# Performance work log

Hardware: AMD Instinct MI355X
Metric: run time of the kernel (lower is better)

Reference implementation:

```python
import jax, jax.numpy as jnp
import numpy as np

N_NODES = 100000
N_EDGES = 1600000
IN_DIM, HID_DIM, OUT_DIM = 128, 64, 16
BN_EPS = 1e-5


def sage_conv(x, edge_index, W_l, b_l, W_r):
    # PyG SAGEConv (aggr='mean'): out = lin_l(mean_j x_j) + lin_r(x_i)
    src, dst = edge_index[0], edge_index[1]
    msgs = x[src]                                   # [E, F] gather
    sums = jax.ops.segment_sum(msgs, dst, num_segments=N_NODES)      # [N, F]
    cnt = jax.ops.segment_sum(jnp.ones((src.shape[0],), x.dtype), dst,
                              num_segments=N_NODES)                  # [N]
    agg = sums / jnp.maximum(cnt, 1.0)[:, None]     # mean; 0 for isolated nodes
    return agg @ W_l.T + b_l + x @ W_r.T


def batchnorm(x, gamma, beta):
    # BatchNorm1d in training mode: normalize over the node (batch) axis
    mean = jnp.mean(x, axis=0)
    var = jnp.var(x, axis=0)
    return (x - mean) * jax.lax.rsqrt(var + BN_EPS) * gamma + beta


def setup_inputs() -> dict:
    key = jax.random.key(0)
    ks = jax.random.split(key, 8)
    x = jax.random.normal(ks[0], (N_NODES, IN_DIM), dtype=jnp.float32)
    edge_index = jax.random.randint(ks[1], (2, N_EDGES), 0, N_NODES)
    s1 = 1.0 / np.sqrt(IN_DIM)
    s2 = 1.0 / np.sqrt(HID_DIM)
    return {
        "x": x,
        "edge_index": edge_index,
        "W1_l": jax.random.uniform(ks[2], (HID_DIM, IN_DIM), minval=-s1, maxval=s1),
        "b1": jnp.zeros((HID_DIM,), jnp.float32),
        "W1_r": jax.random.uniform(ks[3], (HID_DIM, IN_DIM), minval=-s1, maxval=s1),
        "bn_gamma": jnp.ones((HID_DIM,), jnp.float32),
        "bn_beta": jnp.zeros((HID_DIM,), jnp.float32),
        "W2_l": jax.random.uniform(ks[4], (OUT_DIM, HID_DIM), minval=-s2, maxval=s2),
        "b2": jnp.zeros((OUT_DIM,), jnp.float32),
        "W2_r": jax.random.uniform(ks[5], (OUT_DIM, HID_DIM), minval=-s2, maxval=s2),
    }


def reference(x, edge_index, W1_l, b1, W1_r, bn_gamma, bn_beta, W2_l, b2, W2_r):
    h = sage_conv(x, edge_index, W1_l, b1, W1_r)
    h = jax.nn.relu(batchnorm(h, bn_gamma, bn_beta))
    return sage_conv(h, edge_index, W2_l, b2, W2_r)
```

## Files before the change

kernel.cpp:

```cpp
#include <hip/hip_runtime.h>

#define NN 100000
#define NE 1600000
#define NPB 128
#define NBK 782
#define EPB 16384
#define NPART 98
#define NCVT 18
#define NTILES 1563
#define CAP 4096

#define OFF_H      0
#define OFF_GCNT   0
#define OFF_GOFS   80000
#define OFF_W1BF   160000
#define OFF_YL     6400000
#define OFF_YR     9600000
#define OFF_EBUF   12800000
#define OFF_HIST   14400000
#define OFF_BSTART 14500000
#define OFF_BNACC  14500800
#define OFF_W2BF   14500928

typedef __attribute__((ext_vector_type(8))) short bf16x8;
typedef __attribute__((ext_vector_type(4))) float f32x4;

__device__ __forceinline__ ushort f2bf(float f) {
  unsigned u = __float_as_uint(f);
  u += 0x7fffu + ((u >> 16) & 1);
  return (ushort)(u >> 16);
}
#define BFLO(u) __uint_as_float(((u) & 0xffffu) << 16)
#define BFHI(u) __uint_as_float((u) & 0xffff0000u)

__global__ __launch_bounds__(1024) void k_bcnt2(const int* __restrict__ ei,
                                                int* __restrict__ gcnt,
                                                const float* __restrict__ W1l,
                                                const float* __restrict__ W1r,
                                                const float* __restrict__ W2l,
                                                const float* __restrict__ W2r,
                                                ushort* __restrict__ w1bf,
                                                ushort* __restrict__ w2bf) {
  const int tid = threadIdx.x;
  if (blockIdx.x >= NPART) {
    int i = (blockIdx.x - NPART) * 1024 + tid;
    if (i < 16384) {
      w1bf[i] = f2bf(i < 8192 ? W1l[i] : W1r[i - 8192]);
    } else if (i < 16384 + 2048) {
      int j = i - 16384;
      w2bf[j] = f2bf(j < 1024 ? W2l[j] : W2r[j - 1024]);
    }
    return;
  }
  __shared__ int cnt[NBK];
  for (int i = tid; i < NBK; i += 1024) cnt[i] = 0;
  __syncthreads();
  int e0 = blockIdx.x * EPB;
  int e1 = min(e0 + EPB, NE);
  for (int e = e0 + tid; e < e1; e += 1024)
    atomicAdd(&cnt[ei[NE + e] >> 7], 1);
  __syncthreads();
  for (int b = tid; b < NBK; b += 1024)
    gcnt[blockIdx.x * NBK + b] = cnt[b];
}

__global__ __launch_bounds__(1024) void k_bprep(const int* __restrict__ gcnt,
                                                int* __restrict__ bstart,
                                                int* __restrict__ gofs) {
  __shared__ int sd[1024];
  int t = threadIdx.x;
  int total = 0;
  if (t < NBK)
    for (int blk = 0; blk < NPART; ++blk) total += gcnt[blk * NBK + t];
  sd[t] = total;
  __syncthreads();
  for (int off = 1; off < 1024; off <<= 1) {
    int u = (t >= off) ? sd[t - off] : 0;
    __syncthreads();
    sd[t] += u;
    __syncthreads();
  }
  if (t < NBK) {
    int run = sd[t] - total;
    bstart[t] = run;
    for (int blk = 0; blk < NPART; ++blk) {
      gofs[blk * NBK + t] = run;
      run += gcnt[blk * NBK + t];
    }
  }
  if (t == 0) bstart[NBK] = NE;
}

__global__ __launch_bounds__(512) void k_pg(const int* __restrict__ ei,
                                            const int* __restrict__ gofs,
                                            int* __restrict__ ebuf,
                                            const float* __restrict__ x,
                                            const ushort* __restrict__ w1bf,
                                            ushort* __restrict__ yl,
                                            ushort* __restrict__ yr) {
  __shared__ ushort smem[64 * 136];
  const int tid = threadIdx.x;

  if (blockIdx.x < NPART) {
    int* gstart = (int*)smem;
    int* cur = gstart + NBK;
    for (int i = tid; i < NBK; i += 512) {
      gstart[i] = gofs[blockIdx.x * NBK + i];
      cur[i] = 0;
    }
    __syncthreads();
    int e0 = blockIdx.x * EPB;
    int e1 = min(e0 + EPB, NE);
    for (int e = e0 + tid; e < e1; e += 512) {
      int s = ei[e], t = ei[NE + e];
      int b = t >> 7;
      int r = atomicAdd(&cur[b], 1);
      ebuf[gstart[b] + r] = (s << 7) | (t & 127);
    }
    return;
  }

  ushort* xs = smem;
  const int n0 = (blockIdx.x - NPART) * 64;

  for (int i = tid; i < 64 * 32; i += 512) {
    int r = i >> 5, c = i & 31;
    int n = n0 + r;
    float4 v = (n < NN) ? *(const float4*)&x[(size_t)n * 128 + c * 4]
                        : make_float4(0.f, 0.f, 0.f, 0.f);
    *(ushort4*)&xs[r * 136 + c * 4] = make_ushort4(f2bf(v.x), f2bf(v.y), f2bf(v.z), f2bf(v.w));
  }
  __syncthreads();

  const int w = tid >> 6, l = tid & 63;
  const int col = l & 15, kb = l >> 4;

  f32x4 acc[4];
#pragma unroll
  for (int nt = 0; nt < 4; ++nt) acc[nt] = (f32x4){0.f, 0.f, 0.f, 0.f};

#pragma unroll
  for (int kc = 0; kc < 4; ++kc) {
    int koff = kc * 32 + kb * 8;
    bf16x8 a[4];
#pragma unroll
    for (int nt = 0; nt < 4; ++nt)
      a[nt] = *(const bf16x8*)&xs[(nt * 16 + col) * 136 + koff];
    bf16x8 b = *(const bf16x8*)&w1bf[(w * 16 + col) * 128 + koff];
#pragma unroll
    for (int nt = 0; nt < 4; ++nt)
      acc[nt] = __builtin_amdgcn_mfma_f32_16x16x32_bf16(a[nt], b, acc[nt], 0, 0, 0);
  }

  const int outc = w * 16 + col;
#pragma unroll
  for (int nt = 0; nt < 4; ++nt) {
#pragma unroll
    for (int r = 0; r < 4; ++r) {
      int n = n0 + nt * 16 + kb * 4 + r;
      if (n < NN) {
        ushort v = f2bf(acc[nt][r]);
        if (outc < 64) yl[(size_t)n * 64 + outc] = v;
        else           yr[(size_t)n * 64 + (outc - 64)] = v;
      }
    }
  }
}

__global__ __launch_bounds__(512) void k_agg1c(int* __restrict__ ebuf,
                                               const int* __restrict__ bstart,
                                               int* __restrict__ hist,
                                               const ushort* __restrict__ yl,
                                               const ushort* __restrict__ yr,
                                               const float* __restrict__ b1,
                                               float* __restrict__ h,
                                               float* __restrict__ bnacc) {
  __shared__ int raw[CAP];
  __shared__ int srt[CAP];
  __shared__ int sd[128], deg[128], offx[128], cursor[128];
  __shared__ float bnWs[8][64], bnWq[8][64];
  const int tid = threadIdx.x;
  const int b = blockIdx.x;
  const int node0 = b << 7;
  const int nnode = min(NPB, NN - node0);
  const int kstart = bstart[b];
  const int T = min(bstart[b + 1] - kstart, CAP);

  if (tid < 128) deg[tid] = 0;
  __syncthreads();
  for (int i = tid; i < T; i += 512) {
    int e = ebuf[kstart + i];
    raw[i] = e;
    atomicAdd(&deg[e & 127], 1);
  }
  __syncthreads();
  if (tid < 128) sd[tid] = deg[tid];
  __syncthreads();
  for (int o = 1; o < 128; o <<= 1) {
    int v = (tid < 128 && tid >= o) ? sd[tid - o] : 0;
    __syncthreads();
    if (tid < 128) sd[tid] += v;
    __syncthreads();
  }
  if (tid < 128) {
    int s = sd[tid] - deg[tid];
    offx[tid] = s;
    cursor[tid] = s;
    if (tid < nnode) hist[node0 + tid] = deg[tid];
  }
  __syncthreads();

  for (int i = tid; i < T; i += 512) {
    int e = raw[i];
    int slot = atomicAdd(&cursor[e & 127], 1);
    srt[slot] = e >> 7;
  }
  __syncthreads();

  for (int i = tid; i < T; i += 512) ebuf[kstart + i] = srt[i];

  const int g = tid >> 3, f8 = tid & 7;
  float s[8] = {}, q[8] = {};
#pragma unroll
  for (int rep = 0; rep < 2; ++rep) {
    int dl = g + rep * 64;
    if (dl < nnode) {
      int st = offx[dl], d = deg[dl];
      float a[8] = {};
      int k = st, ke = st + d;
      for (; k + 3 < ke; k += 4) {
        int s0 = srt[k], s1 = srt[k + 1], s2 = srt[k + 2], s3 = srt[k + 3];
        uint4 v0 = *(const uint4*)&yl[(size_t)s0 * 64 + f8 * 8];
        uint4 v1 = *(const uint4*)&yl[(size_t)s1 * 64 + f8 * 8];
        uint4 v2 = *(const uint4*)&yl[(size_t)s2 * 64 + f8 * 8];
        uint4 v3 = *(const uint4*)&yl[(size_t)s3 * 64 + f8 * 8];
        a[0] += (BFLO(v0.x) + BFLO(v1.x)) + (BFLO(v2.x) + BFLO(v3.x));
        a[1] += (BFHI(v0.x) + BFHI(v1.x)) + (BFHI(v2.x) + BFHI(v3.x));
        a[2] += (BFLO(v0.y) + BFLO(v1.y)) + (BFLO(v2.y) + BFLO(v3.y));
        a[3] += (BFHI(v0.y) + BFHI(v1.y)) + (BFHI(v2.y) + BFHI(v3.y));
        a[4] += (BFLO(v0.z) + BFLO(v1.z)) + (BFLO(v2.z) + BFLO(v3.z));
        a[5] += (BFHI(v0.z) + BFHI(v1.z)) + (BFHI(v2.z) + BFHI(v3.z));
        a[6] += (BFLO(v0.w) + BFLO(v1.w)) + (BFLO(v2.w) + BFLO(v3.w));
        a[7] += (BFHI(v0.w) + BFHI(v1.w)) + (BFHI(v2.w) + BFHI(v3.w));
      }
      for (; k < ke; ++k) {
        int s0 = srt[k];
        uint4 v0 = *(const uint4*)&yl[(size_t)s0 * 64 + f8 * 8];
        a[0] += BFLO(v0.x); a[1] += BFHI(v0.x);
        a[2] += BFLO(v0.y); a[3] += BFHI(v0.y);
        a[4] += BFLO(v0.z); a[5] += BFHI(v0.z);
        a[6] += BFLO(v0.w); a[7] += BFHI(v0.w);
      }
      int node = node0 + dl;
      float invc = 1.0f / fmaxf((float)d, 1.0f);
      uint4 rv = *(const uint4*)&yr[(size_t)node * 64 + f8 * 8];
      float4 bv0 = *(const float4*)&b1[f8 * 8];
      float4 bv1 = *(const float4*)&b1[f8 * 8 + 4];
      float hv[8];
      hv[0] = a[0] * invc + bv0.x + BFLO(rv.x);
      hv[1] = a[1] * invc + bv0.y + BFHI(rv.x);
      hv[2] = a[2] * invc + bv0.z + BFLO(rv.y);
      hv[3] = a[3] * invc + bv0.w + BFHI(rv.y);
      hv[4] = a[4] * invc + bv1.x + BFLO(rv.z);
      hv[5] = a[5] * invc + bv1.y + BFHI(rv.z);
      hv[6] = a[6] * invc + bv1.z + BFLO(rv.w);
      hv[7] = a[7] * invc + bv1.w + BFHI(rv.w);
      *(float4*)&h[(size_t)node * 64 + f8 * 8]     = make_float4(hv[0], hv[1], hv[2], hv[3]);
      *(float4*)&h[(size_t)node * 64 + f8 * 8 + 4] = make_float4(hv[4], hv[5], hv[6], hv[7]);
#pragma unroll
      for (int j = 0; j < 8; ++j) { s[j] += hv[j]; q[j] += hv[j] * hv[j]; }
    }
  }

#pragma unroll
  for (int j = 0; j < 8; ++j) {
    s[j] += __shfl_xor(s[j], 8);  s[j] += __shfl_xor(s[j], 16); s[j] += __shfl_xor(s[j], 32);
    q[j] += __shfl_xor(q[j], 8);  q[j] += __shfl_xor(q[j], 16); q[j] += __shfl_xor(q[j], 32);
  }
  const int w = tid >> 6, lane = tid & 63;
  if (lane < 8) {
#pragma unroll
    for (int j = 0; j < 8; ++j) {
      bnWs[w][lane * 8 + j] = s[j];
      bnWq[w][lane * 8 + j] = q[j];
    }
  }
  __syncthreads();
  if (tid < 64) {
    float S = 0.f, Q = 0.f;
#pragma unroll
    for (int ww = 0; ww < 8; ++ww) { S += bnWs[ww][tid]; Q += bnWq[ww][tid]; }
    atomicAdd(&bnacc[tid], S);
    atomicAdd(&bnacc[64 + tid], Q);
  }
}

__global__ __launch_bounds__(256) void k_layer2m(const float* __restrict__ h,
                                                 const ushort* __restrict__ w2bf,
                                                 const float* __restrict__ b2,
                                                 const float* __restrict__ bnacc,
                                                 const float* __restrict__ gamma,
                                                 const float* __restrict__ beta,
                                                 ushort* __restrict__ zl,
                                                 float* __restrict__ zr) {
  __shared__ ushort hs[64 * 72];
  __shared__ float sc[64], sh[64];
  const int tid = threadIdx.x;
  const int n0 = blockIdx.x * 64;

  if (tid < 64) {
    float mean = bnacc[tid] * (1.0f / NN);
    float var = bnacc[64 + tid] * (1.0f / NN) - mean * mean;
    float scv = gamma[tid] * rsqrtf(var + 1e-5f);
    sc[tid] = scv;
    sh[tid] = beta[tid] - mean * scv;
  }
  __syncthreads();

  for (int i = tid; i < 64 * 16; i += 256) {
    int r = i >> 4, c = i & 15;
    int n = n0 + r;
    float4 v = (n < NN) ? *(const float4*)&h[(size_t)n * 64 + c * 4]
                        : make_float4(0.f, 0.f, 0.f, 0.f);
    float4 o;
    o.x = fmaxf(v.x * sc[c * 4 + 0] + sh[c * 4 + 0], 0.f);
    o.y = fmaxf(v.y * sc[c * 4 + 1] + sh[c * 4 + 1], 0.f);
    o.z = fmaxf(v.z * sc[c * 4 + 2] + sh[c * 4 + 2], 0.f);
    o.w = fmaxf(v.w * sc[c * 4 + 3] + sh[c * 4 + 3], 0.f);
    *(ushort4*)&hs[r * 72 + c * 4] = make_ushort4(f2bf(o.x), f2bf(o.y), f2bf(o.z), f2bf(o.w));
  }
  __syncthreads();

  const int w = tid >> 6, l = tid & 63;
  const int col = l & 15, kb = l >> 4;

  f32x4 acc[2] = {(f32x4){0.f, 0.f, 0.f, 0.f}, (f32x4){0.f, 0.f, 0.f, 0.f}};
#pragma unroll
  for (int kc = 0; kc < 2; ++kc) {
    int koff = kc * 32 + kb * 8;
    bf16x8 a = *(const bf16x8*)&hs[(w * 16 + col) * 72 + koff];
    bf16x8 b0 = *(const bf16x8*)&w2bf[col * 64 + koff];
    bf16x8 b1v = *(const bf16x8*)&w2bf[(16 + col) * 64 + koff];
    acc[0] = __builtin_amdgcn_mfma_f32_16x16x32_bf16(a, b0, acc[0], 0, 0, 0);
    acc[1] = __builtin_amdgcn_mfma_f32_16x16x32_bf16(a, b1v, acc[1], 0, 0, 0);
  }

#pragma unroll
  for (int r = 0; r < 4; ++r) {
    int n = n0 + w * 16 + kb * 4 + r;
    if (n < NN) {
      zl[(size_t)n * 16 + col] = f2bf(acc[0][r]);
      zr[(size_t)n * 16 + col] = acc[1][r] + b2[col];
    }
  }
}

__global__ __launch_bounds__(512) void k_agg2c(const int* __restrict__ ebuf,
                                               const int* __restrict__ bstart,
                                               const int* __restrict__ hist,
                                               const ushort* __restrict__ zl,
                                               const float* __restrict__ zr,
                                               float* __restrict__ out) {
  __shared__ int elist[CAP];
  __shared__ int sd[128], deg[128], offx[128];
  const int tid = threadIdx.x;
  const int b = blockIdx.x;
  const int node0 = b << 7;
  const int nnode = min(NPB, NN - node0);
  const int kstart = bstart[b];
  const int T = min(bstart[b + 1] - kstart, CAP);

  for (int i = tid; i < T; i += 512) elist[i] = ebuf[kstart + i];
  if (tid < 128) {
    int d = (tid < nnode) ? hist[node0 + tid] : 0;
    deg[tid] = d;
    sd[tid] = d;
  }
  __syncthreads();
  for (int o = 1; o < 128; o <<= 1) {
    int v = (tid < 128 && tid >= o) ? sd[tid - o] : 0;
    __syncthreads();
    if (tid < 128) sd[tid] += v;
    __syncthreads();
  }
  if (tid < 128) offx[tid] = sd[tid] - deg[tid];
  __syncthreads();

  const int g = tid >> 3, f8 = tid & 7;
#pragma unroll
  for (int rep = 0; rep < 2; ++rep) {
    int dl = g + rep * 64;
    if (dl < nnode) {
      int st = offx[dl], d = deg[dl];
      float a0 = 0.f, a1 = 0.f;
      int k = st, ke = st + d;
      for (; k + 3 < ke; k += 4) {
        int s0 = elist[k], s1 = elist[k + 1], s2 = elist[k + 2], s3 = elist[k + 3];
        unsigned v0 = *(const unsigned*)&zl[(size_t)s0 * 16 + f8 * 2];
        unsigned v1 = *(const unsigned*)&zl[(size_t)s1 * 16 + f8 * 2];
        unsigned v2 = *(const unsigned*)&zl[(size_t)s2 * 16 + f8 * 2];
        unsigned v3 = *(const unsigned*)&zl[(size_t)s3 * 16 + f8 * 2];
        a0 += (BFLO(v0) + BFLO(v1)) + (BFLO(v2) + BFLO(v3));
        a1 += (BFHI(v0) + BFHI(v1)) + (BFHI(v2) + BFHI(v3));
      }
      for (; k < ke; ++k) {
        unsigned v0 = *(const unsigned*)&zl[(size_t)elist[k] * 16 + f8 * 2];
        a0 += BFLO(v0);
        a1 += BFHI(v0);
      }
      int node = node0 + dl;
      float invc = 1.0f / fmaxf((float)d, 1.0f);
      size_t base = (size_t)node * 16 + f8 * 2;
      out[base]     = a0 * invc + zr[base];
      out[base + 1] = a1 * invc + zr[base + 1];
    }
  }
}

extern "C" void kernel_launch(void* const* d_in, const int* in_sizes, int n_in,
                              void* d_out, int out_size, void* d_ws, size_t ws_size,
                              hipStream_t stream) {
  const float* x     = (const float*)d_in[0];
  const int*   ei    = (const int*)d_in[1];
  const float* W1l   = (const float*)d_in[2];
  const float* b1    = (const float*)d_in[3];
  const float* W1r   = (const float*)d_in[4];
  const float* gamma = (const float*)d_in[5];
  const float* beta  = (const float*)d_in[6];
  const float* W2l   = (const float*)d_in[7];
  const float* b2    = (const float*)d_in[8];
  const float* W2r   = (const float*)d_in[9];
  float* out = (float*)d_out;
  float* ws  = (float*)d_ws;

  float*  hbuf   = ws + OFF_H;
  int*    gcnt   = (int*)(ws + OFF_GCNT);
  int*    gofs   = (int*)(ws + OFF_GOFS);
  ushort* w1bf   = (ushort*)(ws + OFF_W1BF);
  ushort* yl     = (ushort*)(ws + OFF_YL);
  ushort* yr     = (ushort*)(ws + OFF_YR);
  ushort* zl     = (ushort*)(ws + OFF_YL);
  float*  zr     = ws + OFF_YR;
  int*    ebuf   = (int*)(ws + OFF_EBUF);
  int*    hist   = (int*)(ws + OFF_HIST);
  int*    bstart = (int*)(ws + OFF_BSTART);
  float*  bnacc  = ws + OFF_BNACC;
  ushort* w2bf   = (ushort*)(ws + OFF_W2BF);

  hipMemsetAsync(bnacc, 0, 128 * sizeof(float), stream);

  k_bcnt2<<<NPART + NCVT, 1024, 0, stream>>>(ei, gcnt, W1l, W1r, W2l, W2r, w1bf, w2bf);
  k_bprep<<<1, 1024, 0, stream>>>(gcnt, bstart, gofs);
  k_pg<<<NPART + NTILES, 512, 0, stream>>>(ei, gofs, ebuf, x, w1bf, yl, yr);
  k_agg1c<<<NBK, 512, 0, stream>>>(ebuf, bstart, hist, yl, yr, b1, hbuf, bnacc);
  k_layer2m<<<NTILES, 256, 0, stream>>>(hbuf, w2bf, b2, bnacc, gamma, beta, zl, zr);
  k_agg2c<<<NBK, 512, 0, stream>>>(ebuf, bstart, hist, zl, zr, out);
}
```

Before: 139.5 us.

## Vectorize edge loads, enlarge projection tiles, stage bf16 outputs through LDS

Edge counting and edge partitioning now read four source and destination indices at a time with int4 loads instead of scalar loads. The layer-1 projection tile grows from 64 to 128 nodes per block, which halves the number of tiles and reuses each weight fragment across eight MFMAs. Results are written to shared memory and then stored to yl/yr with coalesced 16-byte writes instead of scattered 2-byte stores. The cost is more LDS and registers per block and fewer blocks to spread across the GPU.

Result: faster. 132.7 us (-4.9%).

```diff
diff --git a/kernel.cpp b/kernel.cpp
--- a/kernel.cpp
+++ b/kernel.cpp
@@ -7,7 +7,8 @@
 #define EPB 16384
 #define NPART 98
 #define NCVT 18
-#define NTILES 1563
+#define NT64 1563
+#define NT128 782
 #define CAP 4096
 
 #define OFF_H      0
@@ -57,8 +58,18 @@
   __syncthreads();
   int e0 = blockIdx.x * EPB;
   int e1 = min(e0 + EPB, NE);
-  for (int e = e0 + tid; e < e1; e += 1024)
-    atomicAdd(&cnt[ei[NE + e] >> 7], 1);
+  for (int base = e0; base < e1; base += 4096) {
+    int e = base + tid * 4;
+    if (e + 3 < e1) {
+      int4 vd = *(const int4*)&ei[NE + e];
+      atomicAdd(&cnt[vd.x >> 7], 1);
+      atomicAdd(&cnt[vd.y >> 7], 1);
+      atomicAdd(&cnt[vd.z >> 7], 1);
+      atomicAdd(&cnt[vd.w >> 7], 1);
+    } else {
+      for (int k = e; k < e1; ++k) atomicAdd(&cnt[ei[NE + k] >> 7], 1);
+    }
+  }
   __syncthreads();
   for (int b = tid; b < NBK; b += 1024)
     gcnt[blockIdx.x * NBK + b] = cnt[b];
@@ -98,7 +109,7 @@
                                             const ushort* __restrict__ w1bf,
                                             ushort* __restrict__ yl,
                                             ushort* __restrict__ yr) {
-  __shared__ ushort smem[64 * 136];
+  __shared__ ushort smem[128 * 136];
   const int tid = threadIdx.x;
 
   if (blockIdx.x < NPART) {
@@ -111,19 +122,36 @@
     __syncthreads();
     int e0 = blockIdx.x * EPB;
     int e1 = min(e0 + EPB, NE);
-    for (int e = e0 + tid; e < e1; e += 512) {
-      int s = ei[e], t = ei[NE + e];
-      int b = t >> 7;
-      int r = atomicAdd(&cur[b], 1);
-      ebuf[gstart[b] + r] = (s << 7) | (t & 127);
+    for (int base = e0; base < e1; base += 2048) {
+      int e = base + tid * 4;
+      if (e + 3 < e1) {
+        int4 vs = *(const int4*)&ei[e];
+        int4 vd = *(const int4*)&ei[NE + e];
+        int b0 = vd.x >> 7, b1 = vd.y >> 7, b2 = vd.z >> 7, b3 = vd.w >> 7;
+        int r0 = atomicAdd(&cur[b0], 1);
+        int r1 = atomicAdd(&cur[b1], 1);
+        int r2 = atomicAdd(&cur[b2], 1);
+        int r3 = atomicAdd(&cur[b3], 1);
+        ebuf[gstart[b0] + r0] = (vs.x << 7) | (vd.x & 127);
+        ebuf[gstart[b1] + r1] = (vs.y << 7) | (vd.y & 127);
+        ebuf[gstart[b2] + r2] = (vs.z << 7) | (vd.z & 127);
+        ebuf[gstart[b3] + r3] = (vs.w << 7) | (vd.w & 127);
+      } else {
+        for (int k = e; k < e1; ++k) {
+          int s = ei[k], d = ei[NE + k];
+          int b = d >> 7;
+          int r = atomicAdd(&cur[b], 1);
+          ebuf[gstart[b] + r] = (s << 7) | (d & 127);
+        }
+      }
     }
     return;
   }
 
   ushort* xs = smem;
-  const int n0 = (blockIdx.x - NPART) * 64;
-
-  for (int i = tid; i < 64 * 32; i += 512) {
+  const int n0 = (blockIdx.x - NPART) * 128;
+
+  for (int i = tid; i < 128 * 32; i += 512) {
     int r = i >> 5, c = i & 31;
     int n = n0 + r;
     float4 v = (n < NN) ? *(const float4*)&x[(size_t)n * 128 + c * 4]
@@ -135,34 +163,37 @@
   const int w = tid >> 6, l = tid & 63;
   const int col = l & 15, kb = l >> 4;
 
-  f32x4 acc[4];
-#pragma unroll
-  for (int nt = 0; nt < 4; ++nt) acc[nt] = (f32x4){0.f, 0.f, 0.f, 0.f};
+  f32x4 acc[8];
+#pragma unroll
+  for (int nt = 0; nt < 8; ++nt) acc[nt] = (f32x4){0.f, 0.f, 0.f, 0.f};
 
 #pragma unroll
   for (int kc = 0; kc < 4; ++kc) {
     int koff = kc * 32 + kb * 8;
-    bf16x8 a[4];
-#pragma unroll
-    for (int nt = 0; nt < 4; ++nt)
-      a[nt] = *(const bf16x8*)&xs[(nt * 16 + col) * 136 + koff];
     bf16x8 b = *(const bf16x8*)&w1bf[(w * 16 + col) * 128 + koff];
 #pragma unroll
-    for (int nt = 0; nt < 4; ++nt)
-      acc[nt] = __builtin_amdgcn_mfma_f32_16x16x32_bf16(a[nt], b, acc[nt], 0, 0, 0);
-  }
-
+    for (int nt = 0; nt < 8; ++nt) {
+      bf16x8 a = *(const bf16x8*)&xs[(nt * 16 + col) * 136 + koff];
+      acc[nt] = __builtin_amdgcn_mfma_f32_16x16x32_bf16(a, b, acc[nt], 0, 0, 0);
+    }
+  }
+
+  __syncthreads();
   const int outc = w * 16 + col;
 #pragma unroll
-  for (int nt = 0; nt < 4; ++nt) {
-#pragma unroll
-    for (int r = 0; r < 4; ++r) {
-      int n = n0 + nt * 16 + kb * 4 + r;
-      if (n < NN) {
-        ushort v = f2bf(acc[nt][r]);
-        if (outc < 64) yl[(size_t)n * 64 + outc] = v;
-        else           yr[(size_t)n * 64 + (outc - 64)] = v;
-      }
+  for (int nt = 0; nt < 8; ++nt)
+#pragma unroll
+    for (int r = 0; r < 4; ++r)
+      xs[(nt * 16 + kb * 4 + r) * 136 + outc] = f2bf(acc[nt][r]);
+  __syncthreads();
+
+  for (int i = tid; i < 2048; i += 512) {
+    int row = i >> 4, seg = i & 15;
+    int n = n0 + row;
+    if (n < NN) {
+      uint4 v = *(const uint4*)&xs[row * 136 + seg * 8];
+      if (seg < 8) *(uint4*)&yl[(size_t)n * 64 + seg * 8] = v;
+      else         *(uint4*)&yr[(size_t)n * 64 + (seg - 8) * 8] = v;
     }
   }
 }
@@ -451,8 +482,8 @@
 
   k_bcnt2<<<NPART + NCVT, 1024, 0, stream>>>(ei, gcnt, W1l, W1r, W2l, W2r, w1bf, w2bf);
   k_bprep<<<1, 1024, 0, stream>>>(gcnt, bstart, gofs);
-  k_pg<<<NPART + NTILES, 512, 0, stream>>>(ei, gofs, ebuf, x, w1bf, yl, yr);
+  k_pg<<<NPART + NT128, 512, 0, stream>>>(ei, gofs, ebuf, x, w1bf, yl, yr);
   k_agg1c<<<NBK, 512, 0, stream>>>(ebuf, bstart, hist, yl, yr, b1, hbuf, bnacc);
-  k_layer2m<<<NTILES, 256, 0, stream>>>(hbuf, w2bf, b2, bnacc, gamma, beta, zl, zr);
+  k_layer2m<<<NT64, 256, 0, stream>>>(hbuf, w2bf, b2, bnacc, gamma, beta, zl, zr);
   k_agg2c<<<NBK, 512, 0, stream>>>(ebuf, bstart, hist, zl, zr, out);
 }
```
